# Kernel optimization log

Hardware: AMD Instinct MI355X
Metric: run time of the kernel (lower is better)

Reference implementation:

```python
import jax, jax.numpy as jnp
import numpy as np

N = 512
D = 400          # per-sample feature dim (lstm_hidden_dim * 2)
H = 400          # hidden dim of F_func (lstm_hidden_dim * 2)


def setup_inputs() -> dict:
    key = jax.random.key(0)
    k1, k2, k3, k4, k5, k6 = jax.random.split(key, 6)
    x_samples = jax.random.normal(k1, (N, D), dtype=jnp.float32)
    y_samples = jax.random.normal(k2, (N, D), dtype=jnp.float32)
    # torch nn.Linear default init: U(-1/sqrt(fan_in), 1/sqrt(fan_in))
    b1_bound = 1.0 / np.sqrt(2 * D)
    b2_bound = 1.0 / np.sqrt(H)
    W1 = jax.random.uniform(k3, (H, 2 * D), minval=-b1_bound, maxval=b1_bound, dtype=jnp.float32)
    b1 = jax.random.uniform(k4, (H,), minval=-b1_bound, maxval=b1_bound, dtype=jnp.float32)
    W2 = jax.random.uniform(k5, (1, H), minval=-b2_bound, maxval=b2_bound, dtype=jnp.float32)
    b2 = jax.random.uniform(k6, (1,), minval=-b2_bound, maxval=b2_bound, dtype=jnp.float32)
    return {"x_samples": x_samples, "y_samples": y_samples,
            "W1": W1, "b1": b1, "W2": W2, "b2": b2}


def reference(x_samples, y_samples, W1, b1, W2, b2):
    n = y_samples.shape[0]
    W1x, W1y = W1[:, :D], W1[:, D:]
    hx = x_samples @ W1x.T          # [N, H], contribution of x
    hy = y_samples @ W1y.T          # [N, H], contribution of y

    def score(h):  # second linear + softplus, squeeze out last dim of 1
        return jax.nn.softplus(h @ W2.T + b2)[..., 0]

    # T0[i] = F(x[i], y[i])
    T0 = score(jax.nn.relu(hx + hy + b1))                      # [N]
    # T1[i, j] = F(x[j], y[i])  (x tiled along dim 0, y along dim 1)
    h_pair = jax.nn.relu(hy[:, None, :] + hx[None, :, :] + b1) # [N, N, H]
    T1 = score(h_pair)                                          # [N, N]

    t0_mean = T0.mean()
    lower_bound = t0_mean - (jax.nn.logsumexp(T1, axis=1).mean() - jnp.log(jnp.float32(n)))
    upper_bound = t0_mean - T1.mean()
    return (lower_bound, upper_bound)
```

## Files before the change

### kernel.cpp

```cpp
#include <hip/hip_runtime.h>
#include <math.h>


#define NSAMP 512
#define DIM 400
#define HID 400

__global__ __launch_bounds__(512) void club_gemm_kernel(
    const float* __restrict__ X, const float* __restrict__ Y,
    const float* __restrict__ W1, const float* __restrict__ b1,
    float* __restrict__ hxT0, float* __restrict__ hxT1,
    float* __restrict__ hyb0, float* __restrict__ hyb1)
{
    __shared__ float As[64 * 105];
    __shared__ float Bs[64 * 105];
    const int t  = threadIdx.x;
    const int tx = t & 15;
    const int ty = t >> 4;
    const int n0 = blockIdx.x * 64;
    const int h0 = blockIdx.y * 64;
    const int z  = blockIdx.z;
    const int mat = z >> 1, kh = z & 1;
    const float* __restrict__ src = mat ? Y : X;
    const int wcol0 = (mat ? DIM : 0) + kh * 200;
    const int scol0 = kh * 200;

    float acc[4][2];
#pragma unroll
    for (int c = 0; c < 4; c++) { acc[c][0] = 0.f; acc[c][1] = 0.f; }

    for (int kc = 0; kc < 200; kc += 100) {
        __syncthreads();
        for (int idx = t; idx < 1600; idx += 512) {
            int n = idx / 25, k4 = idx % 25;
            float4 v = *(const float4*)(src + (size_t)(n0 + n) * DIM + scol0 + kc + 4 * k4);
            float* d = As + n * 105 + 4 * k4;
            d[0] = v.x; d[1] = v.y; d[2] = v.z; d[3] = v.w;
        }
        for (int idx = t; idx < 1600; idx += 512) {
            int h = idx / 25, k4 = idx % 25;
            int hrow = h0 + h; if (hrow > HID - 1) hrow = HID - 1;
            float4 v = *(const float4*)(W1 + (size_t)hrow * (2 * DIM) + wcol0 + kc + 4 * k4);
            float* d = Bs + h * 105 + 4 * k4;
            d[0] = v.x; d[1] = v.y; d[2] = v.z; d[3] = v.w;
        }
        __syncthreads();
#pragma unroll 4
        for (int k = 0; k < 100; k++) {
            float a0 = As[(2 * ty + 0) * 105 + k];
            float a1 = As[(2 * ty + 1) * 105 + k];
#pragma unroll
            for (int c = 0; c < 4; c++) {
                float b = Bs[(4 * tx + c) * 105 + k];
                acc[c][0] = fmaf(a0, b, acc[c][0]);
                acc[c][1] = fmaf(a1, b, acc[c][1]);
            }
        }
    }

    if ((h0 + 4 * tx) < HID) {
        if (mat == 0) {
            float* __restrict__ dst = kh ? hxT1 : hxT0;
#pragma unroll
            for (int c = 0; c < 4; c++) {
                int h = h0 + 4 * tx + c;
                *(float2*)(dst + (size_t)h * NSAMP + n0 + 2 * ty) =
                    make_float2(acc[c][0], acc[c][1]);
            }
        } else {
            float* __restrict__ dst = kh ? hyb1 : hyb0;
            if (kh == 0) {
                float4 bv = *(const float4*)(b1 + h0 + 4 * tx);
                acc[0][0] += bv.x; acc[0][1] += bv.x;
                acc[1][0] += bv.y; acc[1][1] += bv.y;
                acc[2][0] += bv.z; acc[2][1] += bv.z;
                acc[3][0] += bv.w; acc[3][1] += bv.w;
            }
#pragma unroll
            for (int r = 0; r < 2; r++) {
                int n = n0 + 2 * ty + r;
                *(float4*)(dst + (size_t)n * HID + h0 + 4 * tx) =
                    make_float4(acc[0][r], acc[1][r], acc[2][r], acc[3][r]);
            }
        }
    }
}

__global__ __launch_bounds__(256) void club_pair_kernel(
    const float* __restrict__ hxT0, const float* __restrict__ hxT1,
    const float* __restrict__ hyb0, const float* __restrict__ hyb1,
    const float* __restrict__ W2, const float* __restrict__ b2,
    double* __restrict__ expsum, double* __restrict__ tsum,
    double* __restrict__ diagT)
{
    __shared__ float As[16 * 204];
    __shared__ float Bs[200 * 32];
    const int t  = threadIdx.x;
    const int tx = t & 31;
    const int ty = t >> 5;
    const int i0 = blockIdx.x * 16;
    const int j0 = blockIdx.y * 32;
    const int j  = j0 + tx;

    float acc[2] = {0.f, 0.f};

    for (int hc = 0; hc < HID; hc += 200) {
        __syncthreads();
        for (int idx = t; idx < 800; idx += 256) {
            int i = idx / 50, q = idx % 50;
            size_t off = (size_t)(i0 + i) * HID + hc + 4 * q;
            float4 v0 = *(const float4*)(hyb0 + off);
            float4 v1 = *(const float4*)(hyb1 + off);
            *(float4*)(As + i * 204 + 4 * q) =
                make_float4(v0.x + v1.x, v0.y + v1.y, v0.z + v1.z, v0.w + v1.w);
        }
        for (int idx = t; idx < 1600; idx += 256) {
            int h = idx >> 3, q = idx & 7;
            size_t off = (size_t)(hc + h) * NSAMP + j0 + 4 * q;
            float4 v0 = *(const float4*)(hxT0 + off);
            float4 v1 = *(const float4*)(hxT1 + off);
            *(float4*)(Bs + h * 32 + 4 * q) =
                make_float4(v0.x + v1.x, v0.y + v1.y, v0.z + v1.z, v0.w + v1.w);
        }
        __syncthreads();
        const float* __restrict__ w2p = W2 + hc;
#pragma unroll 8
        for (int h = 0; h < 200; h++) {
            float w  = w2p[h];
            float b  = Bs[h * 32 + tx];
            float a0 = As[(2 * ty + 0) * 204 + h];
            float a1 = As[(2 * ty + 1) * 204 + h];
            acc[0] = fmaf(fmaxf(a0 + b, 0.f), w, acc[0]);
            acc[1] = fmaf(fmaxf(a1 + b, 0.f), w, acc[1]);
        }
    }

    const float bb2 = b2[0];
#pragma unroll
    for (int r = 0; r < 2; r++) {
        const int i = i0 + 2 * ty + r;
        float s  = acc[r] + bb2;
        float es = expf(s);
        float T  = log1pf(es);
        if (j == i) diagT[i] = (double)T;
        double eD = 1.0 + (double)es;
        double tD = (double)T;
        for (int off = 16; off > 0; off >>= 1) {
            eD += __shfl_down(eD, off);
            tD += __shfl_down(tD, off);
        }
        if (tx == 0) {
            expsum[i * 16 + blockIdx.y] = eD;
            tsum  [i * 16 + blockIdx.y] = tD;
        }
    }
}

__global__ __launch_bounds__(512) void club_final_kernel(
    const double* __restrict__ expsum, const double* __restrict__ tsum,
    const double* __restrict__ diagT, float* __restrict__ out)
{
    __shared__ double sh[3 * 512];
    const int t = threadIdx.x;
    double es = 0.0, ts = 0.0;
#pragma unroll
    for (int b = 0; b < 16; b++) { es += expsum[t * 16 + b]; ts += tsum[t * 16 + b]; }
    sh[t] = log(es); sh[512 + t] = ts; sh[1024 + t] = diagT[t];
    __syncthreads();
    for (int off = 256; off > 0; off >>= 1) {
        if (t < off) {
            sh[t]        += sh[t + off];
            sh[512 + t]  += sh[512 + t + off];
            sh[1024 + t] += sh[1024 + t + off];
        }
        __syncthreads();
    }
    if (t == 0) {
        double t0m  = sh[1024] / 512.0;
        double lsem = sh[0]    / 512.0;
        double t1m  = sh[512]  / (512.0 * 512.0);
        out[0] = (float)(t0m - (lsem - log(512.0)));
        out[1] = (float)(t0m - t1m);
    }
}

extern "C" void kernel_launch(void* const* d_in, const int* in_sizes, int n_in,
                              void* d_out, int out_size, void* d_ws, size_t ws_size,
                              hipStream_t stream) {
    const float* X  = (const float*)d_in[0];
    const float* Y  = (const float*)d_in[1];
    const float* W1 = (const float*)d_in[2];
    const float* b1 = (const float*)d_in[3];
    const float* W2 = (const float*)d_in[4];
    const float* b2 = (const float*)d_in[5];
    float* out = (float*)d_out;

    char* ws = (char*)d_ws;
    float*  hxT0   = (float*) (ws);
    float*  hxT1   = (float*) (ws +  819200);
    float*  hyb0   = (float*) (ws + 1638400);
    float*  hyb1   = (float*) (ws + 2457600);
    double* expsum = (double*)(ws + 3276800);
    double* tsum   = (double*)(ws + 3342336);
    double* diagT  = (double*)(ws + 3407872);

    club_gemm_kernel <<<dim3(8, 7, 4), 512, 0, stream>>>(X, Y, W1, b1, hxT0, hxT1, hyb0, hyb1);
    club_pair_kernel <<<dim3(32, 16),  256, 0, stream>>>(hxT0, hxT1, hyb0, hyb1, W2, b2,
                                                         expsum, tsum, diagT);
    club_final_kernel<<<1, 512, 0, stream>>>(expsum, tsum, diagT, out);
}
```

Measured before the change: 115.3 us.

## Fuse three kernels into one cooperative kernel with grid syncs

Merges the projection GEMM, pairwise score, and final reduction kernels into a single cooperative launch of 256 blocks of 1024 threads, separated by grid.sync barriers, so two kernel launches and their gaps go away. The shared-memory tiles are transposed for float2/float4 vector reads, each thread computes a 2x2 or single output instead of the earlier mappings, and W2 is staged in shared memory. The cost is grid-wide barriers, lower per-thread work in the pair stage, and reliance on every block being co-resident.

```diff
diff --git a/kernel.cpp b/kernel.cpp
--- a/kernel.cpp
+++ b/kernel.cpp
@@ -1,148 +1,152 @@
 #include <hip/hip_runtime.h>
+#include <hip/hip_cooperative_groups.h>
 #include <math.h>
+
+namespace cg = cooperative_groups;
 
 
 #define NSAMP 512
 #define DIM 400
 #define HID 400
 
-__global__ __launch_bounds__(512) void club_gemm_kernel(
+__global__ __launch_bounds__(1024, 4) void club_fused(
     const float* __restrict__ X, const float* __restrict__ Y,
     const float* __restrict__ W1, const float* __restrict__ b1,
+    const float* __restrict__ W2, const float* __restrict__ b2,
     float* __restrict__ hxT0, float* __restrict__ hxT1,
-    float* __restrict__ hyb0, float* __restrict__ hyb1)
+    float* __restrict__ hyb0, float* __restrict__ hyb1,
+    double* __restrict__ expsum, double* __restrict__ tsum,
+    double* __restrict__ diagT, float* __restrict__ out)
 {
-    __shared__ float As[64 * 105];
-    __shared__ float Bs[64 * 105];
-    const int t  = threadIdx.x;
-    const int tx = t & 15;
-    const int ty = t >> 4;
-    const int n0 = blockIdx.x * 64;
-    const int h0 = blockIdx.y * 64;
-    const int z  = blockIdx.z;
-    const int mat = z >> 1, kh = z & 1;
-    const float* __restrict__ src = mat ? Y : X;
-    const int wcol0 = (mat ? DIM : 0) + kh * 200;
-    const int scol0 = kh * 200;
-
-    float acc[4][2];
-#pragma unroll
-    for (int c = 0; c < 4; c++) { acc[c][0] = 0.f; acc[c][1] = 0.f; }
-
-    for (int kc = 0; kc < 200; kc += 100) {
-        __syncthreads();
-        for (int idx = t; idx < 1600; idx += 512) {
-            int n = idx / 25, k4 = idx % 25;
-            float4 v = *(const float4*)(src + (size_t)(n0 + n) * DIM + scol0 + kc + 4 * k4);
-            float* d = As + n * 105 + 4 * k4;
-            d[0] = v.x; d[1] = v.y; d[2] = v.z; d[3] = v.w;
-        }
-        for (int idx = t; idx < 1600; idx += 512) {
-            int h = idx / 25, k4 = idx % 25;
-            int hrow = h0 + h; if (hrow > HID - 1) hrow = HID - 1;
-            float4 v = *(const float4*)(W1 + (size_t)hrow * (2 * DIM) + wcol0 + kc + 4 * k4);
-            float* d = Bs + h * 105 + 4 * k4;
-            d[0] = v.x; d[1] = v.y; d[2] = v.z; d[3] = v.w;
-        }
-        __syncthreads();
+    __shared__ __align__(16) float W2s[400];
+    __shared__ __align__(16) float U[13200];
+    cg::grid_group grid = cg::this_grid();
+
+    const int t   = threadIdx.x;
+    const int blk = blockIdx.x;
+    if (t < 400) W2s[t] = W2[t];
+
+    if (blk < 224) {
+        const int mat = blk & 1, kh = (blk >> 1) & 1, rem = blk >> 2;
+        const int h7 = rem % 7, n8 = rem / 7;
+        const float* __restrict__ src = mat ? Y : X;
+        const int n0 = n8 * 64, h0 = h7 * 64;
+        const int scol = kh * 200;
+        const int wcol = (mat ? DIM : 0) + kh * 200;
+        const int lo = t & 31, hi = t >> 5;
+        const int n2 = mat ? hi : lo;
+        const int h2 = mat ? lo : hi;
+
+        float* As = U;
+        float* Bs = U + 6600;
+
+        float a00 = 0.f, a01 = 0.f, a10 = 0.f, a11 = 0.f;
+
+        for (int kc = 0; kc < 200; kc += 100) {
+            __syncthreads();
+            for (int idx = t; idx < 1600; idx += 1024) {
+                int n = idx / 25, q = idx - n * 25;
+                float4 v = *(const float4*)(src + (size_t)(n0 + n) * DIM + scol + kc + 4 * q);
+                int base = 4 * q * 66 + n;
+                As[base] = v.x; As[base + 66] = v.y; As[base + 132] = v.z; As[base + 198] = v.w;
+            }
+            for (int idx = t; idx < 1600; idx += 1024) {
+                int h = idx / 25, q = idx - h * 25;
+                int hr = h0 + h; if (hr > HID - 1) hr = HID - 1;
+                float4 v = *(const float4*)(W1 + (size_t)hr * (2 * DIM) + wcol + kc + 4 * q);
+                int base = 4 * q * 66 + h;
+                Bs[base] = v.x; Bs[base + 66] = v.y; Bs[base + 132] = v.z; Bs[base + 198] = v.w;
+            }
+            __syncthreads();
 #pragma unroll 4
-        for (int k = 0; k < 100; k++) {
-            float a0 = As[(2 * ty + 0) * 105 + k];
-            float a1 = As[(2 * ty + 1) * 105 + k];
-#pragma unroll
-            for (int c = 0; c < 4; c++) {
-                float b = Bs[(4 * tx + c) * 105 + k];
-                acc[c][0] = fmaf(a0, b, acc[c][0]);
-                acc[c][1] = fmaf(a1, b, acc[c][1]);
-            }
-        }
-    }
-
-    if ((h0 + 4 * tx) < HID) {
+            for (int k = 0; k < 100; k++) {
+                float2 av = *(const float2*)(As + k * 66 + 2 * n2);
+                float2 bv = *(const float2*)(Bs + k * 66 + 2 * h2);
+                a00 = fmaf(av.x, bv.x, a00);
+                a01 = fmaf(av.x, bv.y, a01);
+                a10 = fmaf(av.y, bv.x, a10);
+                a11 = fmaf(av.y, bv.y, a11);
+            }
+        }
+
         if (mat == 0) {
             float* __restrict__ dst = kh ? hxT1 : hxT0;
-#pragma unroll
-            for (int c = 0; c < 4; c++) {
-                int h = h0 + 4 * tx + c;
-                *(float2*)(dst + (size_t)h * NSAMP + n0 + 2 * ty) =
-                    make_float2(acc[c][0], acc[c][1]);
-            }
+            const int n = n0 + 2 * lo, h = h0 + 2 * hi;
+            if (h < HID)     *(float2*)(dst + (size_t)h * NSAMP + n)       = make_float2(a00, a10);
+            if (h + 1 < HID) *(float2*)(dst + (size_t)(h + 1) * NSAMP + n) = make_float2(a01, a11);
         } else {
             float* __restrict__ dst = kh ? hyb1 : hyb0;
-            if (kh == 0) {
-                float4 bv = *(const float4*)(b1 + h0 + 4 * tx);
-                acc[0][0] += bv.x; acc[0][1] += bv.x;
-                acc[1][0] += bv.y; acc[1][1] += bv.y;
-                acc[2][0] += bv.z; acc[2][1] += bv.z;
-                acc[3][0] += bv.w; acc[3][1] += bv.w;
-            }
-#pragma unroll
-            for (int r = 0; r < 2; r++) {
-                int n = n0 + 2 * ty + r;
-                *(float4*)(dst + (size_t)n * HID + h0 + 4 * tx) =
-                    make_float4(acc[0][r], acc[1][r], acc[2][r], acc[3][r]);
+            const int h = h0 + 2 * lo, n = n0 + 2 * hi;
+            if (h < HID) {
+                float2 v0 = make_float2(a00, a01);
+                float2 v1 = make_float2(a10, a11);
+                if (kh == 0) {
+                    float2 bv = *(const float2*)(b1 + h);
+                    v0.x += bv.x; v0.y += bv.y; v1.x += bv.x; v1.y += bv.y;
+                }
+                *(float2*)(dst + (size_t)n * HID + h)       = v0;
+                *(float2*)(dst + (size_t)(n + 1) * HID + h) = v1;
             }
         }
     }
-}
-
-__global__ __launch_bounds__(256) void club_pair_kernel(
-    const float* __restrict__ hxT0, const float* __restrict__ hxT1,
-    const float* __restrict__ hyb0, const float* __restrict__ hyb1,
-    const float* __restrict__ W2, const float* __restrict__ b2,
-    double* __restrict__ expsum, double* __restrict__ tsum,
-    double* __restrict__ diagT)
-{
-    __shared__ float As[16 * 204];
-    __shared__ float Bs[200 * 32];
-    const int t  = threadIdx.x;
-    const int tx = t & 31;
-    const int ty = t >> 5;
-    const int i0 = blockIdx.x * 16;
-    const int j0 = blockIdx.y * 32;
-    const int j  = j0 + tx;
-
-    float acc[2] = {0.f, 0.f};
-
-    for (int hc = 0; hc < HID; hc += 200) {
-        __syncthreads();
-        for (int idx = t; idx < 800; idx += 256) {
-            int i = idx / 50, q = idx % 50;
-            size_t off = (size_t)(i0 + i) * HID + hc + 4 * q;
-            float4 v0 = *(const float4*)(hyb0 + off);
-            float4 v1 = *(const float4*)(hyb1 + off);
-            *(float4*)(As + i * 204 + 4 * q) =
-                make_float4(v0.x + v1.x, v0.y + v1.y, v0.z + v1.z, v0.w + v1.w);
-        }
-        for (int idx = t; idx < 1600; idx += 256) {
-            int h = idx >> 3, q = idx & 7;
-            size_t off = (size_t)(hc + h) * NSAMP + j0 + 4 * q;
-            float4 v0 = *(const float4*)(hxT0 + off);
-            float4 v1 = *(const float4*)(hxT1 + off);
-            *(float4*)(Bs + h * 32 + 4 * q) =
-                make_float4(v0.x + v1.x, v0.y + v1.y, v0.z + v1.z, v0.w + v1.w);
-        }
-        __syncthreads();
-        const float* __restrict__ w2p = W2 + hc;
-#pragma unroll 8
-        for (int h = 0; h < 200; h++) {
-            float w  = w2p[h];
-            float b  = Bs[h * 32 + tx];
-            float a0 = As[(2 * ty + 0) * 204 + h];
-            float a1 = As[(2 * ty + 1) * 204 + h];
-            acc[0] = fmaf(fmaxf(a0 + b, 0.f), w, acc[0]);
-            acc[1] = fmaf(fmaxf(a1 + b, 0.f), w, acc[1]);
-        }
-    }
-
-    const float bb2 = b2[0];
-#pragma unroll
-    for (int r = 0; r < 2; r++) {
-        const int i = i0 + 2 * ty + r;
-        float s  = acc[r] + bb2;
+
+    __threadfence();
+    grid.sync();
+
+    {
+        const int half = t >> 9;
+        const int tt   = t & 511;
+        const int job  = blk * 2 + half;
+        const int it = job >> 4, jt = job & 15;
+        const int i0 = it * 16, j0 = jt * 32;
+        const int tx = tt & 31;
+        const int ty = tt >> 5;
+        float* Ah = U + half * 5184;
+        float* Bh = U + half * 5184 + 16 * 108;
+
+        float acc = 0.f;
+        for (int hc = 0; hc < HID; hc += 100) {
+            __syncthreads();
+            for (int idx = tt; idx < 400; idx += 512) {
+                int i = idx / 25, q = idx - i * 25;
+                size_t off = (size_t)(i0 + i) * HID + hc + 4 * q;
+                float4 v0 = *(const float4*)(hyb0 + off);
+                float4 v1 = *(const float4*)(hyb1 + off);
+                *(float4*)(Ah + i * 108 + 4 * q) =
+                    make_float4(v0.x + v1.x, v0.y + v1.y, v0.z + v1.z, v0.w + v1.w);
+            }
+            for (int idx = tt; idx < 800; idx += 512) {
+                int h = idx >> 3, jq = idx & 7;
+                size_t off = (size_t)(hc + h) * NSAMP + j0 + 4 * jq;
+                float4 v0 = *(const float4*)(hxT0 + off);
+                float4 v1 = *(const float4*)(hxT1 + off);
+                float* d = Bh + (4 * jq) * 108 + h;
+                d[0]   = v0.x + v1.x;
+                d[108] = v0.y + v1.y;
+                d[216] = v0.z + v1.z;
+                d[324] = v0.w + v1.w;
+            }
+            __syncthreads();
+            const float* ap = Ah + ty * 108;
+            const float* bp = Bh + tx * 108;
+            const float* wp = W2s + hc;
+#pragma unroll 5
+            for (int g = 0; g < 25; g++) {
+                float4 av = *(const float4*)(ap + 4 * g);
+                float4 bv = *(const float4*)(bp + 4 * g);
+                float4 wv = *(const float4*)(wp + 4 * g);
+                acc = fmaf(fmaxf(av.x + bv.x, 0.f), wv.x, acc);
+                acc = fmaf(fmaxf(av.y + bv.y, 0.f), wv.y, acc);
+                acc = fmaf(fmaxf(av.z + bv.z, 0.f), wv.z, acc);
+                acc = fmaf(fmaxf(av.w + bv.w, 0.f), wv.w, acc);
+            }
+        }
+
+        const int i = i0 + ty, j = j0 + tx;
+        float s  = acc + b2[0];
         float es = expf(s);
         float T  = log1pf(es);
-        if (j == i) diagT[i] = (double)T;
+        if (i == j) diagT[i] = (double)T;
         double eD = 1.0 + (double)es;
         double tD = (double)T;
         for (int off = 16; off > 0; off >>= 1) {
@@ -150,37 +154,41 @@
             tD += __shfl_down(tD, off);
         }
         if (tx == 0) {
-            expsum[i * 16 + blockIdx.y] = eD;
-            tsum  [i * 16 + blockIdx.y] = tD;
+            expsum[i * 16 + jt] = eD;
+            tsum  [i * 16 + jt] = tD;
         }
     }
-}
-
-__global__ __launch_bounds__(512) void club_final_kernel(
-    const double* __restrict__ expsum, const double* __restrict__ tsum,
-    const double* __restrict__ diagT, float* __restrict__ out)
-{
-    __shared__ double sh[3 * 512];
-    const int t = threadIdx.x;
-    double es = 0.0, ts = 0.0;
+
+    __threadfence();
+    grid.sync();
+
+    if (blk == 0) {
+        double* sh = (double*)U;
+        double lse = 0.0, tsm = 0.0, dg = 0.0;
+        if (t < 512) {
+            double es = 0.0, ts = 0.0;
 #pragma unroll
-    for (int b = 0; b < 16; b++) { es += expsum[t * 16 + b]; ts += tsum[t * 16 + b]; }
-    sh[t] = log(es); sh[512 + t] = ts; sh[1024 + t] = diagT[t];
-    __syncthreads();
-    for (int off = 256; off > 0; off >>= 1) {
-        if (t < off) {
-            sh[t]        += sh[t + off];
-            sh[512 + t]  += sh[512 + t + off];
-            sh[1024 + t] += sh[1024 + t + off];
+            for (int b = 0; b < 16; b++) { es += expsum[t * 16 + b]; ts += tsum[t * 16 + b]; }
+            lse = log(es); tsm = ts; dg = diagT[t];
         }
         __syncthreads();
-    }
-    if (t == 0) {
-        double t0m  = sh[1024] / 512.0;
-        double lsem = sh[0]    / 512.0;
-        double t1m  = sh[512]  / (512.0 * 512.0);
-        out[0] = (float)(t0m - (lsem - log(512.0)));
-        out[1] = (float)(t0m - t1m);
+        if (t < 512) { sh[t] = lse; sh[512 + t] = tsm; sh[1024 + t] = dg; }
+        __syncthreads();
+        for (int off = 256; off > 0; off >>= 1) {
+            if (t < off) {
+                sh[t]        += sh[t + off];
+                sh[512 + t]  += sh[512 + t + off];
+                sh[1024 + t] += sh[1024 + t + off];
+            }
+            __syncthreads();
+        }
+        if (t == 0) {
+            double t0m  = sh[1024] / 512.0;
+            double lsem = sh[0]    / 512.0;
+            double t1m  = sh[512]  / (512.0 * 512.0);
+            out[0] = (float)(t0m - (lsem - log(512.0)));
+            out[1] = (float)(t0m - t1m);
+        }
     }
 }
 
@@ -204,8 +212,9 @@
     double* tsum   = (double*)(ws + 3342336);
     double* diagT  = (double*)(ws + 3407872);
 
-    club_gemm_kernel <<<dim3(8, 7, 4), 512, 0, stream>>>(X, Y, W1, b1, hxT0, hxT1, hyb0, hyb1);
-    club_pair_kernel <<<dim3(32, 16),  256, 0, stream>>>(hxT0, hxT1, hyb0, hyb1, W2, b2,
-                                                         expsum, tsum, diagT);
-    club_final_kernel<<<1, 512, 0, stream>>>(expsum, tsum, diagT, out);
+    void* args[] = { (void*)&X, (void*)&Y, (void*)&W1, (void*)&b1, (void*)&W2, (void*)&b2,
+                     (void*)&hxT0, (void*)&hxT1, (void*)&hyb0, (void*)&hyb1,
+                     (void*)&expsum, (void*)&tsum, (void*)&diagT, (void*)&out };
+    hipLaunchCooperativeKernel((const void*)club_fused, dim3(256), dim3(1024),
+                               args, 0, stream);
 }
```

New measurement: 338.1 us. 193% more time.
